# Kernel tuning notes

Measured on AMD Instinct MI355X. Metric: run time of the kernel, lower is better.

Reference implementation:

```python
import jax, jax.numpy as jnp
import numpy as np

D = 1024      # d_model
H = 16        # heads
KD = 64       # per-head dim
STRIDE = 64   # local chunk size
LH = 8        # local heads
GH = H - LH   # global heads
C = 4         # attended positions per global head per chunk


def setup_inputs() -> dict:
    key = jax.random.key(0)
    ks = jax.random.split(key, 12)
    B, S = 4, 4096
    sc = 1.0 / np.sqrt(D)
    x = jax.random.normal(ks[0], (B, S, D), jnp.float32)
    input_mask = jax.random.randint(ks[1], (B, S), 0, 2).astype(bool)
    Wq = jax.random.normal(ks[2], (D, D), jnp.float32) * sc
    bq = jax.random.normal(ks[3], (D,), jnp.float32) * 0.01
    Wk = jax.random.normal(ks[4], (D, D), jnp.float32) * sc
    bk = jax.random.normal(ks[5], (D,), jnp.float32) * 0.01
    Wv = jax.random.normal(ks[6], (D, D), jnp.float32) * sc
    bv = jax.random.normal(ks[7], (D,), jnp.float32) * 0.01
    Wo = jax.random.normal(ks[8], (D, D), jnp.float32) * sc
    bo = jax.random.normal(ks[9], (D,), jnp.float32) * 0.01
    return {"x": x, "input_mask": input_mask, "Wq": Wq, "bq": bq,
            "Wk": Wk, "bk": bk, "Wv": Wv, "bv": bv, "Wo": Wo, "bo": bo}


def reference(x, input_mask, Wq, bq, Wk, bk, Wv, bv, Wo, bo):
    B, S, _ = x.shape
    q = (x @ Wq.T + bq).reshape(B, S, H, KD)
    k = (x @ Wk.T + bk).reshape(B, S, H, KD)
    v = (x @ Wv.T + bv).reshape(B, S, H, KD)

    # ---- local heads: per the original code, the local attention scores are
    # computed but discarded; local_qkv = chunk_local_value reshaped back,
    # which is exactly the (head-major) local values. We reproduce that math.
    local_qkv = jnp.transpose(v[:, :, :LH, :], (0, 2, 1, 3))  # (B, LH, S, KD)

    # ---- global heads: each global head attends, inside every chunk, to a
    # fixed window of C positions near the end of the chunk.
    nc = S // STRIDE
    start = STRIDE - GH * C
    base = jnp.arange(start, STRIDE).reshape(GH, C)          # (GH, C)
    offs = jnp.arange(0, S, STRIDE)                          # (nc,)
    idx = (base[:, None, :] + offs[None, :, None]).reshape(GH, nc * C)  # (GH, L)
    L = nc * C

    gq = jnp.transpose(q[:, :, LH:, :], (0, 2, 1, 3))        # (B, GH, S, KD)
    gk = jnp.transpose(k[:, :, LH:, :], (0, 2, 1, 3))
    gv = jnp.transpose(v[:, :, LH:, :], (0, 2, 1, 3))

    h_idx = jnp.arange(GH)[:, None]                          # (GH, 1)
    gk_sel = gk[:, h_idx, idx, :]                            # (B, GH, L, KD)
    gv_sel = gv[:, h_idx, idx, :]                            # (B, GH, L, KD)

    qk = jnp.einsum('bhsd,bhld->bhsl', gq, gk_sel) * (KD ** -0.5)
    gmask = input_mask[:, idx]                               # (B, GH, L)
    qk = jnp.where(gmask[:, :, None, :], jnp.float32(-1e10), qk)
    attn = jax.nn.softmax(qk, axis=-1)
    g_out = jnp.einsum('bhsl,bhld->bhsd', attn, gv_sel)      # (B, GH, S, KD)

    qkv = jnp.concatenate([local_qkv, g_out], axis=1)        # (B, H, S, KD)
    qkv = jnp.transpose(qkv, (0, 2, 1, 3)).reshape(B, S, H * KD)
    return qkv @ Wo.T + bo
```

## Files before the change

kernel.cpp:

```cpp
#include <hip/hip_runtime.h>
#include <stdint.h>


typedef __bf16 bf16_t;
typedef __bf16 bf16x4 __attribute__((ext_vector_type(4)));
typedef __bf16 bf16x8 __attribute__((ext_vector_type(8)));
typedef float floatx4 __attribute__((ext_vector_type(4)));

#define MFMA16(a, b, c) __builtin_amdgcn_mfma_f32_16x16x32_bf16((a), (b), (c), 0, 0, 0)

__device__ __forceinline__ void glds16(const bf16_t* g, const bf16_t* lds_base) {
  __builtin_amdgcn_global_load_lds(
      (const __attribute__((address_space(1))) uint32_t*)(uintptr_t)g,
      (__attribute__((address_space(3))) uint32_t*)(uintptr_t)lds_base, 16, 0, 0);
}

#define VMCNT(n)  asm volatile("s_waitcnt vmcnt(" #n ")" ::: "memory")
#define LGKMCNT0  asm volatile("s_waitcnt lgkmcnt(0)" ::: "memory")
#define SBAR      __builtin_amdgcn_s_barrier()
#define SCHED0    __builtin_amdgcn_sched_barrier(0)

__global__ void cvt_f32_bf16(const float* __restrict__ src, bf16_t* __restrict__ dst, int n) {
  const int i = (blockIdx.x * 256 + threadIdx.x) * 4;
  if (i < n) {
    float4 v = *(const float4*)(src + i);
    bf16x4 d = {(bf16_t)v.x, (bf16_t)v.y, (bf16_t)v.z, (bf16_t)v.w};
    *(bf16x4*)(dst + i) = d;
  }
}

__global__ void pack_bias(const float* __restrict__ bv, const float* __restrict__ bq,
                          const float* __restrict__ bk, float* __restrict__ bcat) {
  const int i = blockIdx.x * 256 + threadIdx.x;
  float v;
  if (i < 1024) v = bv[i];
  else if (i < 1536) v = bq[i - 512];
  else v = bk[i - 1024];
  bcat[i] = v;
}

#define G8_SETUP(A_, W_, ROW0_, COL0_)                                          \
  __shared__ bf16_t As[2][16384];                                               \
  __shared__ bf16_t Bs[2][16384];                                               \
  const int tid = threadIdx.x;                                                  \
  const int w = tid >> 6, l = tid & 63;                                         \
  const int lq = l >> 4, lm = l & 15;                                           \
  const int wr = (w >> 2) << 7;                      \
  const int wc = (w & 3) << 6;                \
  const long row0 = (ROW0_);                                                    \
  const long col0 = (COL0_);                                                    \
  floatx4 acc[8][4];                                                            \
  { floatx4 z = {0.f, 0.f, 0.f, 0.f};                                           \
    _Pragma("unroll") for (int i = 0; i < 8; ++i)                               \
    _Pragma("unroll") for (int j = 0; j < 4; ++j) acc[i][j] = z; }              \
  const int t7 = tid & 127, t8 = tid >> 7;                                      \
  const bf16_t* pAt = (A_) + (row0 + t7) * 1024 + t8 * 8;                       \
  const bf16_t* pBt = (W_) + (col0 + t7) * 1024 + t8 * 8;                       \
  const int sbase = ((((w >> 1) << 8) + ((w & 1) << 6)) << 3);

#define G8_ST_A(s, off, jk)                                                     \
  glds16(pAt + (off),          &As[s][0] + ((jk) << 13) + sbase);               \
  glds16(pAt + 131072 + (off), &As[s][0] + ((jk) << 13) + 1024 + sbase);
#define G8_ST_B(s, off, jk)                                                     \
  glds16(pBt + (off),          &Bs[s][0] + ((jk) << 13) + sbase);               \
  glds16(pBt + 131072 + (off), &Bs[s][0] + ((jk) << 13) + 1024 + sbase);

#define G8_READ_B(s, kk)                                                        \
  _Pragma("unroll") for (int nt = 0; nt < 4; ++nt)                              \
    bfr[nt] = *(const bf16x8*)(&Bs[s][0] +                                      \
        (((((kk) * 4 + lq) << 8) + wc + nt * 16 + lm) << 3));

#define G8_READ_A(s, kk, mh)                                                    \
  _Pragma("unroll") for (int i = 0; i < 4; ++i)                                 \
    af[i] = *(const bf16x8*)(&As[s][0] +                                        \
        (((((kk) * 4 + lq) << 8) + wr + (mh) * 64 + i * 16 + lm) << 3));

#define G8_MFMA(mh)                                                             \
  __builtin_amdgcn_s_setprio(1);                                                \
  _Pragma("unroll") for (int i = 0; i < 4; ++i)                                 \
    _Pragma("unroll") for (int nt = 0; nt < 4; ++nt)                            \
      acc[(mh) * 4 + i][nt] = MFMA16(af[i], bfr[nt], acc[(mh) * 4 + i][nt]);    \
  __builtin_amdgcn_s_setprio(0);

#define PH_PRE   SCHED0; SBAR; LGKMCNT0; SCHED0;
#define PH_POST  SCHED0; SBAR; SCHED0;

#define G8_ITER                                                                 \
                                                                       \
    G8_READ_A(0, 0, 0) G8_READ_B(0, 0)                                          \
    G8_ST_A(1, 96, 1)                                                           \
    PH_PRE G8_MFMA(0) PH_POST                                                   \
                                                                       \
    G8_READ_A(0, 0, 1)                                                          \
    G8_ST_B(1, 96, 1)                                                           \
    VMCNT(4);                                                                   \
    PH_PRE G8_MFMA(1) PH_POST                                                   \
                                                                       \
    G8_READ_A(0, 1, 0) G8_READ_B(0, 1)                                          \
    G8_ST_A(0, 128, 0)                                                          \
    PH_PRE G8_MFMA(0) PH_POST                                                   \
                                                                       \
    G8_READ_A(0, 1, 1)                                                          \
    G8_ST_B(0, 128, 0)                                                          \
    PH_PRE G8_MFMA(1) PH_POST                                                   \
                                                                       \
    G8_READ_A(1, 0, 0) G8_READ_B(1, 0)                                          \
    G8_ST_A(0, 160, 1)                                                          \
    PH_PRE G8_MFMA(0) PH_POST                                                   \
                                                                       \
    G8_READ_A(1, 0, 1)                                                          \
    G8_ST_B(0, 160, 1)                                                          \
    VMCNT(8);                                                                   \
    PH_PRE G8_MFMA(1) PH_POST                                                   \
                                                                       \
    G8_READ_A(1, 1, 0) G8_READ_B(1, 1)                                          \
    G8_ST_A(1, 192, 0)                                                          \
    PH_PRE G8_MFMA(0) PH_POST                                                   \
                                                                       \
    G8_READ_A(1, 1, 1)                                                          \
    G8_ST_B(1, 192, 0)                                                          \
    VMCNT(8);                                                                   \
    PH_PRE G8_MFMA(1) PH_POST

#define G8_TAIL                                                                 \
    G8_READ_A(0, 0, 0) G8_READ_B(0, 0)                                          \
    G8_ST_A(1, 96, 1)                                                           \
    PH_PRE G8_MFMA(0) PH_POST                                                   \
    G8_READ_A(0, 0, 1)                                                          \
    G8_ST_B(1, 96, 1)                                                           \
    VMCNT(4);                                                                   \
    PH_PRE G8_MFMA(1) PH_POST                                                   \
    G8_READ_A(0, 1, 0) G8_READ_B(0, 1)                                          \
    PH_PRE G8_MFMA(0) PH_POST                                                   \
    G8_READ_A(0, 1, 1)                                                          \
    PH_PRE G8_MFMA(1) PH_POST                                                   \
    G8_READ_A(1, 0, 0) G8_READ_B(1, 0)                                          \
    PH_PRE G8_MFMA(0) PH_POST                                                   \
    G8_READ_A(1, 0, 1)                                                          \
    VMCNT(0);                                                                   \
    PH_PRE G8_MFMA(1) PH_POST                                                   \
    G8_READ_A(1, 1, 0) G8_READ_B(1, 1)                                          \
    PH_PRE G8_MFMA(0) PH_POST                                                   \
    G8_READ_A(1, 1, 1)                                                          \
    PH_PRE G8_MFMA(1) PH_POST

#define G8_MAIN                                                                 \
  G8_ST_A(0, 0, 0) G8_ST_B(0, 0, 0)                                             \
  G8_ST_A(0, 32, 1) G8_ST_B(0, 32, 1)                                           \
  G8_ST_A(1, 64, 0) G8_ST_B(1, 64, 0)                                           \
  VMCNT(0); SBAR; SCHED0;                                                       \
  bf16x8 af[4], bfr[4];                                                         \
  for (int t = 0; t < 7; ++t) {                                                 \
    G8_ITER                                                                     \
    pAt += 128; pBt += 128;                                                     \
  }                                                                             \
  G8_TAIL

__global__ __launch_bounds__(512, 2)
void gemm_bt(const bf16_t* __restrict__ A, const bf16_t* __restrict__ W,
             const float* __restrict__ bias, float* __restrict__ C, int ldc) {
  const int n = blockIdx.x, xcd = n & 7, j = n >> 3;
  G8_SETUP(A, W, (long)(xcd * 8 + (j & 7)) * 256, (long)(j >> 3) * 256)
  G8_MAIN
#pragma unroll
  for (int nt = 0; nt < 4; ++nt) {
    const long col = col0 + wc + nt * 16 + lm;
    const float bc = bias[col];
#pragma unroll
    for (int mt = 0; mt < 8; ++mt) {
#pragma unroll
      for (int r = 0; r < 4; ++r) {
        const long row = row0 + wr + mt * 16 + lq * 4 + r;
        C[row * (long)ldc + col] = acc[mt][nt][r] + bc;
      }
    }
  }
}

__global__ __launch_bounds__(512, 2)
void gemm_proj(const bf16_t* __restrict__ A, const bf16_t* __restrict__ Wcat,
               const float* __restrict__ bcat, bf16_t* __restrict__ qkv,
               bf16_t* __restrict__ vg, bf16_t* __restrict__ qg,
               bf16_t* __restrict__ kg) {
  const int n = blockIdx.x, xcd = n & 7, j = n >> 3;
  G8_SETUP(A, Wcat, (long)(xcd * 8 + (j & 7)) * 256, (long)(j >> 3) * 256)
  G8_MAIN
  bf16_t* dst; long ld, cofs;
  if (col0 < 512)       { dst = qkv; ld = 1024; cofs = 0; }
  else if (col0 < 1024) { dst = vg;  ld = 512;  cofs = 512; }
  else if (col0 < 1536) { dst = qg;  ld = 512;  cofs = 1024; }
  else                  { dst = kg;  ld = 512;  cofs = 1536; }
#pragma unroll
  for (int nt = 0; nt < 4; ++nt) {
    const long col = col0 + wc + nt * 16 + lm;
    const float bc = bcat[col];
    const long cl = col - cofs;
#pragma unroll
    for (int mt = 0; mt < 8; ++mt) {
#pragma unroll
      for (int r = 0; r < 4; ++r) {
        const long row = row0 + wr + mt * 16 + lq * 4 + r;
        dst[row * ld + cl] = (bf16_t)(acc[mt][nt][r] + bc);
      }
    }
  }
}

__global__ __launch_bounds__(256, 1)
void attn_sparse(const bf16_t* __restrict__ qg, const bf16_t* __restrict__ kg,
                 const bf16_t* __restrict__ vg, const int* __restrict__ mask,
                 bf16_t* __restrict__ qkv) {
  __shared__ bf16_t Ks[16384];
  __shared__ bf16_t Vt[64 * 264];
  __shared__ bf16_t Ps[4 * 16 * 136];
  __shared__ int smask[256];

  const int tid = threadIdx.x;
  const int b = blockIdx.z, h = blockIdx.y, qt = blockIdx.x;

  {
    const int lk = tid;
    const int token = ((lk >> 2) << 6) + 32 + (h << 2) + (lk & 3);
    const size_t rowi = (size_t)(b * 4096 + token);
    const uint4* ksrc = (const uint4*)(kg + rowi * 512 + h * 64);
#pragma unroll
    for (int kq = 0; kq < 8; ++kq)
      *(uint4*)(Ks + (kq * 256 + lk) * 8) = ksrc[kq];
    const bf16_t* vsrc = vg + rowi * 512 + h * 64;
#pragma unroll
    for (int i = 0; i < 8; ++i) {
      bf16x8 vv = *(const bf16x8*)(vsrc + i * 8);
#pragma unroll
      for (int j = 0; j < 8; ++j) Vt[(i * 8 + j) * 264 + lk] = vv[j];
    }
    smask[lk] = mask[b * 4096 + token];
  }
  __syncthreads();

  const int w = tid >> 6, l = tid & 63, lq = l >> 4, lm = l & 15;
  const int mrow = (qt << 6) + (w << 4);

  const bf16_t* qrow = qg + (size_t)(b * 4096 + mrow + lm) * 512 + h * 64 + lq * 8;
  bf16x8 aq0 = *(const bf16x8*)qrow;
  bf16x8 aq1 = *(const bf16x8*)(qrow + 32);

  floatx4 zero4 = {0.f, 0.f, 0.f, 0.f};
  floatx4 s[16];
#pragma unroll
  for (int t = 0; t < 16; ++t) {
    bf16x8 kb0 = *(const bf16x8*)(Ks + (lq * 256 + t * 16 + lm) * 8);
    bf16x8 kb1 = *(const bf16x8*)(Ks + ((4 + lq) * 256 + t * 16 + lm) * 8);
    floatx4 z = zero4;
    z = MFMA16(aq0, kb0, z);
    z = MFMA16(aq1, kb1, z);
    s[t] = z;
  }

  float rmax[4] = {-1e30f, -1e30f, -1e30f, -1e30f};
#pragma unroll
  for (int t = 0; t < 16; ++t) {
    const bool mk = smask[t * 16 + lm] != 0;
#pragma unroll
    for (int r = 0; r < 4; ++r) {
      float v = s[t][r] * 0.125f;
      v = mk ? -1e10f : v;
      s[t][r] = v;
      rmax[r] = fmaxf(rmax[r], v);
    }
  }
#pragma unroll
  for (int off = 1; off < 16; off <<= 1)
#pragma unroll
    for (int r = 0; r < 4; ++r) rmax[r] = fmaxf(rmax[r], __shfl_xor(rmax[r], off));
  float rsum[4] = {0.f, 0.f, 0.f, 0.f};
#pragma unroll
  for (int t = 0; t < 16; ++t)
#pragma unroll
    for (int r = 0; r < 4; ++r) {
      float p = __expf(s[t][r] - rmax[r]);
      s[t][r] = p;
      rsum[r] += p;
    }
#pragma unroll
  for (int off = 1; off < 16; off <<= 1)
#pragma unroll
    for (int r = 0; r < 4; ++r) rsum[r] += __shfl_xor(rsum[r], off);
  float rinv[4];
#pragma unroll
  for (int r = 0; r < 4; ++r) rinv[r] = 1.0f / rsum[r];

  floatx4 o[4];
#pragma unroll
  for (int dt = 0; dt < 4; ++dt) o[dt] = zero4;
  bf16_t* Pw = Ps + w * (16 * 136);
#pragma unroll
  for (int half = 0; half < 2; ++half) {
#pragma unroll
    for (int t = 0; t < 8; ++t) {
      const int tt = half * 8 + t;
#pragma unroll
      for (int r = 0; r < 4; ++r)
        Pw[(lq * 4 + r) * 136 + t * 16 + lm] = (bf16_t)(s[tt][r] * rinv[r]);
    }
    __syncthreads();
#pragma unroll
    for (int ks = 0; ks < 4; ++ks) {
      bf16x8 pa = *(const bf16x8*)(Pw + lm * 136 + ks * 32 + lq * 8);
#pragma unroll
      for (int dt = 0; dt < 4; ++dt) {
        bf16x8 vb = *(const bf16x8*)(Vt + (dt * 16 + lm) * 264 + half * 128 + ks * 32 + lq * 8);
        o[dt] = MFMA16(pa, vb, o[dt]);
      }
    }
    __syncthreads();
  }

#pragma unroll
  for (int dt = 0; dt < 4; ++dt) {
    const int d = dt * 16 + lm;
#pragma unroll
    for (int r = 0; r < 4; ++r) {
      const int token = mrow + lq * 4 + r;
      qkv[(size_t)(b * 4096 + token) * 1024 + 512 + h * 64 + d] = (bf16_t)o[dt][r];
    }
  }
}

extern "C" void kernel_launch(void* const* d_in, const int* in_sizes, int n_in,
                              void* d_out, int out_size, void* d_ws, size_t ws_size,
                              hipStream_t stream) {
  const float* x   = (const float*)d_in[0];
  const int* mask  = (const int*)d_in[1];
  const float* Wq  = (const float*)d_in[2];
  const float* bq  = (const float*)d_in[3];
  const float* Wk  = (const float*)d_in[4];
  const float* bk  = (const float*)d_in[5];
  const float* Wv  = (const float*)d_in[6];
  const float* bv  = (const float*)d_in[7];
  const float* Wo  = (const float*)d_in[8];
  const float* bo  = (const float*)d_in[9];
  float* out = (float*)d_out;

  char* ws = (char*)d_ws;
  bf16_t* xb   = (bf16_t*)(ws);
  bf16_t* Wcat = (bf16_t*)(ws + 33554432L);
  bf16_t* Wob  = (bf16_t*)(ws + 37748736L);
  float*  bcat = (float*)(ws + 39845888L);
  bf16_t* vg   = (bf16_t*)(ws + 39854080L);
  bf16_t* qg   = (bf16_t*)(ws + 56631296L);
  bf16_t* kg   = (bf16_t*)(ws + 73408512L);
  bf16_t* qkv  = (bf16_t*)(ws + 90185728L);

  dim3 blk(256);
  cvt_f32_bf16<<<16384, blk, 0, stream>>>(x, xb, 16777216);
  cvt_f32_bf16<<<1024, blk, 0, stream>>>(Wv, Wcat, 1048576);
  cvt_f32_bf16<<<512, blk, 0, stream>>>(Wq + 524288, Wcat + 1048576, 524288);
  cvt_f32_bf16<<<512, blk, 0, stream>>>(Wk + 524288, Wcat + 1572864, 524288);
  cvt_f32_bf16<<<1024, blk, 0, stream>>>(Wo, Wob, 1048576);
  pack_bias<<<8, blk, 0, stream>>>(bv, bq, bk, bcat);

  gemm_proj<<<512, dim3(512), 0, stream>>>(xb, Wcat, bcat, qkv, vg, qg, kg);
  attn_sparse<<<dim3(64, 8, 4), dim3(256), 0, stream>>>(qg, kg, vg, mask, qkv);
  gemm_bt<<<256, dim3(512), 0, stream>>>(qkv, Wob, bo, out, 1024);
}
```

Baseline: 369.0 us.

## Project global K/V only at attended token positions inside a fused projection GEMM

The projection GEMM now splits its blocks into two groups. The first group computes local V and global Q for all tokens. The second group gathers only the rows of x at positions 32–63 of each 64-token chunk and computes global V and K just for those, writing them into compact buffers that the attention kernel indexes by compressed row. This removes projection FLOPs and K/V writes for tokens that are never attended. The block-to-tile mapping of the output GEMM is also reshuffled. The cost is a gathered, irregular A-load path, and the 384-block grid gives uneven occupancy across CUs.

Measured after the change: 363.9 us. About the same (-1.4%).

```diff
diff --git a/kernel.cpp b/kernel.cpp
--- a/kernel.cpp
+++ b/kernel.cpp
@@ -39,7 +39,7 @@
   bcat[i] = v;
 }
 
-#define G8_SETUP(A_, W_, ROW0_, COL0_)                                          \
+#define G8_DECL                                                                 \
   __shared__ bf16_t As[2][16384];                                               \
   __shared__ bf16_t Bs[2][16384];                                               \
   const int tid = threadIdx.x;                                                  \
@@ -47,20 +47,16 @@
   const int lq = l >> 4, lm = l & 15;                                           \
   const int wr = (w >> 2) << 7;                      \
   const int wc = (w & 3) << 6;                \
-  const long row0 = (ROW0_);                                                    \
-  const long col0 = (COL0_);                                                    \
   floatx4 acc[8][4];                                                            \
   { floatx4 z = {0.f, 0.f, 0.f, 0.f};                                           \
     _Pragma("unroll") for (int i = 0; i < 8; ++i)                               \
     _Pragma("unroll") for (int j = 0; j < 4; ++j) acc[i][j] = z; }              \
   const int t7 = tid & 127, t8 = tid >> 7;                                      \
-  const bf16_t* pAt = (A_) + (row0 + t7) * 1024 + t8 * 8;                       \
-  const bf16_t* pBt = (W_) + (col0 + t7) * 1024 + t8 * 8;                       \
   const int sbase = ((((w >> 1) << 8) + ((w & 1) << 6)) << 3);
 
 #define G8_ST_A(s, off, jk)                                                     \
-  glds16(pAt + (off),          &As[s][0] + ((jk) << 13) + sbase);               \
-  glds16(pAt + 131072 + (off), &As[s][0] + ((jk) << 13) + 1024 + sbase);
+  glds16(pAt + (off),         &As[s][0] + ((jk) << 13) + sbase);                \
+  glds16(pAt + aoff2 + (off), &As[s][0] + ((jk) << 13) + 1024 + sbase);
 #define G8_ST_B(s, off, jk)                                                     \
   glds16(pBt + (off),          &Bs[s][0] + ((jk) << 13) + sbase);               \
   glds16(pBt + 131072 + (off), &Bs[s][0] + ((jk) << 13) + 1024 + sbase);
@@ -86,37 +82,29 @@
 #define PH_POST  SCHED0; SBAR; SCHED0;
 
 #define G8_ITER                                                                 \
-                                                                       \
     G8_READ_A(0, 0, 0) G8_READ_B(0, 0)                                          \
     G8_ST_A(1, 96, 1)                                                           \
     PH_PRE G8_MFMA(0) PH_POST                                                   \
-                                                                       \
     G8_READ_A(0, 0, 1)                                                          \
     G8_ST_B(1, 96, 1)                                                           \
     VMCNT(4);                                                                   \
     PH_PRE G8_MFMA(1) PH_POST                                                   \
-                                                                       \
     G8_READ_A(0, 1, 0) G8_READ_B(0, 1)                                          \
     G8_ST_A(0, 128, 0)                                                          \
     PH_PRE G8_MFMA(0) PH_POST                                                   \
-                                                                       \
     G8_READ_A(0, 1, 1)                                                          \
     G8_ST_B(0, 128, 0)                                                          \
     PH_PRE G8_MFMA(1) PH_POST                                                   \
-                                                                       \
     G8_READ_A(1, 0, 0) G8_READ_B(1, 0)                                          \
     G8_ST_A(0, 160, 1)                                                          \
     PH_PRE G8_MFMA(0) PH_POST                                                   \
-                                                                       \
     G8_READ_A(1, 0, 1)                                                          \
     G8_ST_B(0, 160, 1)                                                          \
     VMCNT(8);                                                                   \
     PH_PRE G8_MFMA(1) PH_POST                                                   \
-                                                                       \
     G8_READ_A(1, 1, 0) G8_READ_B(1, 1)                                          \
     G8_ST_A(1, 192, 0)                                                          \
     PH_PRE G8_MFMA(0) PH_POST                                                   \
-                                                                       \
     G8_READ_A(1, 1, 1)                                                          \
     G8_ST_B(1, 192, 0)                                                          \
     VMCNT(8);                                                                   \
@@ -157,33 +145,35 @@
   G8_TAIL
 
 __global__ __launch_bounds__(512, 2)
-void gemm_bt(const bf16_t* __restrict__ A, const bf16_t* __restrict__ W,
-             const float* __restrict__ bias, float* __restrict__ C, int ldc) {
-  const int n = blockIdx.x, xcd = n & 7, j = n >> 3;
-  G8_SETUP(A, W, (long)(xcd * 8 + (j & 7)) * 256, (long)(j >> 3) * 256)
-  G8_MAIN
-#pragma unroll
-  for (int nt = 0; nt < 4; ++nt) {
-    const long col = col0 + wc + nt * 16 + lm;
-    const float bc = bias[col];
-#pragma unroll
-    for (int mt = 0; mt < 8; ++mt) {
-#pragma unroll
-      for (int r = 0; r < 4; ++r) {
-        const long row = row0 + wr + mt * 16 + lq * 4 + r;
-        C[row * (long)ldc + col] = acc[mt][nt][r] + bc;
-      }
-    }
-  }
-}
-
-__global__ __launch_bounds__(512, 2)
-void gemm_proj(const bf16_t* __restrict__ A, const bf16_t* __restrict__ Wcat,
-               const float* __restrict__ bcat, bf16_t* __restrict__ qkv,
-               bf16_t* __restrict__ vg, bf16_t* __restrict__ qg,
-               bf16_t* __restrict__ kg) {
-  const int n = blockIdx.x, xcd = n & 7, j = n >> 3;
-  G8_SETUP(A, Wcat, (long)(xcd * 8 + (j & 7)) * 256, (long)(j >> 3) * 256)
+void gemm_fused(const bf16_t* __restrict__ A, const bf16_t* __restrict__ Wcat,
+                const float* __restrict__ bcat, bf16_t* __restrict__ qkv,
+                bf16_t* __restrict__ vg, bf16_t* __restrict__ qg,
+                bf16_t* __restrict__ kg) {
+  G8_DECL
+  const int n = blockIdx.x;
+  long row0, col0;
+  int aoff2;
+  const bf16_t* pAt;
+  if (n < 256) {
+    const int xcd = n & 7;
+    const int ct = xcd >> 1;
+    row0 = (long)(((n >> 3) << 1) | (xcd & 1)) * 256;
+    col0 = ct * 256 + (ct >= 2 ? 512 : 0);
+    aoff2 = 131072;
+    pAt = A + (row0 + t7) * 1024 + t8 * 8;
+  } else {
+    const int m2 = n - 256;
+    const int xcd = m2 & 7;
+    const int ct = xcd >> 1;
+    row0 = (long)(((m2 >> 3) << 1) | (xcd & 1)) * 256;
+    col0 = (ct < 2) ? (512 + ct * 256) : (1536 + (ct - 2) * 256);
+    aoff2 = 262144;
+    long r = row0 + t7;
+    if (r > 8063) r = 8063;
+    const long g = ((r >> 5) << 6) + 32 + (r & 31);
+    pAt = A + g * 1024 + t8 * 8;
+  }
+  const bf16_t* pBt = Wcat + (col0 + t7) * 1024 + t8 * 8;
   G8_MAIN
   bf16_t* dst; long ld, cofs;
   if (col0 < 512)       { dst = qkv; ld = 1024; cofs = 0; }
@@ -201,6 +191,32 @@
       for (int r = 0; r < 4; ++r) {
         const long row = row0 + wr + mt * 16 + lq * 4 + r;
         dst[row * ld + cl] = (bf16_t)(acc[mt][nt][r] + bc);
+      }
+    }
+  }
+}
+
+__global__ __launch_bounds__(512, 2)
+void gemm_bt(const bf16_t* __restrict__ A, const bf16_t* __restrict__ W,
+             const float* __restrict__ bias, float* __restrict__ C, int ldc) {
+  G8_DECL
+  const int n = blockIdx.x, xcd = n & 7;
+  const long row0 = (long)(((n >> 3) << 1) | (xcd & 1)) * 256;
+  const long col0 = (long)(xcd >> 1) * 256;
+  const int aoff2 = 131072;
+  const bf16_t* pAt = A + (row0 + t7) * 1024 + t8 * 8;
+  const bf16_t* pBt = W + (col0 + t7) * 1024 + t8 * 8;
+  G8_MAIN
+#pragma unroll
+  for (int nt = 0; nt < 4; ++nt) {
+    const long col = col0 + wc + nt * 16 + lm;
+    const float bc = bias[col];
+#pragma unroll
+    for (int mt = 0; mt < 8; ++mt) {
+#pragma unroll
+      for (int r = 0; r < 4; ++r) {
+        const long row = row0 + wr + mt * 16 + lq * 4 + r;
+        C[row * (long)ldc + col] = acc[mt][nt][r] + bc;
       }
     }
   }
@@ -221,7 +237,8 @@
   {
     const int lk = tid;
     const int token = ((lk >> 2) << 6) + 32 + (h << 2) + (lk & 3);
-    const size_t rowi = (size_t)(b * 4096 + token);
+    const int selrow = ((lk >> 2) << 5) + (h << 2) + (lk & 3);
+    const size_t rowi = (size_t)(b * 2048 + selrow);
     const uint4* ksrc = (const uint4*)(kg + rowi * 512 + h * 64);
 #pragma unroll
     for (int kq = 0; kq < 8; ++kq)
@@ -359,7 +376,7 @@
   cvt_f32_bf16<<<1024, blk, 0, stream>>>(Wo, Wob, 1048576);
   pack_bias<<<8, blk, 0, stream>>>(bv, bq, bk, bcat);
 
-  gemm_proj<<<512, dim3(512), 0, stream>>>(xb, Wcat, bcat, qkv, vg, qg, kg);
+  gemm_fused<<<384, dim3(512), 0, stream>>>(xb, Wcat, bcat, qkv, vg, qg, kg);
   attn_sparse<<<dim3(64, 8, 4), dim3(256), 0, stream>>>(qg, kg, vg, mask, qkv);
   gemm_bt<<<256, dim3(512), 0, stream>>>(qkv, Wob, bo, out, 1024);
 }
```
